# Optimization experiments

Hardware: AMD Instinct MI355X
Metric: run time of the kernel (lower is better)

Reference implementation:

```python
import jax, jax.numpy as jnp
import numpy as np

N_NODES = 100000
N_EDGES = 1600000
IN_CH = 128
OUT_CH = 128

def setup_inputs() -> dict:
    key = jax.random.key(0)
    k1, k2, k3, k4, k5 = jax.random.split(key, 5)
    x = jax.random.normal(k1, (N_NODES, IN_CH), dtype=jnp.float32)
    src = jax.random.randint(k2, (N_EDGES,), 0, N_NODES, dtype=jnp.int64)
    dst = jax.random.randint(k3, (N_EDGES,), 0, N_NODES, dtype=jnp.int64)
    edge_index = jnp.stack([src, dst], axis=0)
    W = jax.random.normal(k4, (OUT_CH, IN_CH), dtype=jnp.float32) * (1.0 / np.sqrt(IN_CH))
    b = jax.random.normal(k5, (OUT_CH,), dtype=jnp.float32) * 0.01
    return {"x": x, "edge_index": edge_index, "W": W, "b": b}

def reference(x, edge_index, W, b):
    n = x.shape[0]
    src, dst = edge_index[0], edge_index[1]
    loop = jnp.arange(n, dtype=edge_index.dtype)
    src_all = jnp.concatenate([src, loop])  # [E+N]
    dst_all = jnp.concatenate([dst, loop])  # [E+N]
    # in-degree (with self loops) per node
    deg = jax.ops.segment_sum(jnp.ones_like(dst_all, dtype=x.dtype), dst_all, num_segments=n)
    norm = (deg[src_all] * deg[dst_all]) ** -0.5
    norm = jnp.where(jnp.isinf(norm), 0.0, norm)
    h = x @ W.T + b  # [N, out_ch]
    msg = h[src_all] * norm[:, None]  # [E+N, out_ch]
    out = jax.ops.segment_sum(msg, dst_all, num_segments=n)  # [N, out_ch]
    return out
```

## Files before the change

### kernel.cpp

```cpp
#include <hip/hip_runtime.h>
#include <hip/hip_bf16.h>


#define N_NODES 100000
#define N_EDGES 1600000
#define CH 128
#define NC 49
#define NBLKA 782
#define CAPC 34816
#define NCHUNK 17
#define NFB 1563
#define FCAP 1280

using bf16x8 = __attribute__((ext_vector_type(8))) short;
using f32x4  = __attribute__((ext_vector_type(4))) float;

__device__ inline unsigned short f2bf(float f) {
    unsigned u = __float_as_uint(f);
    u += 0x7fffu + ((u >> 16) & 1u);
    return (unsigned short)(u >> 16);
}
__device__ inline float bflo(unsigned u) { return __uint_as_float(u << 16); }
__device__ inline float bfhi(unsigned u) { return __uint_as_float(u & 0xffff0000u); }

__global__ __launch_bounds__(256) void k_histA(const int* __restrict__ dst,
                                               int* __restrict__ histG) {
    __shared__ int hist[NC];
    const int t    = threadIdx.x;
    const int base = blockIdx.x * 2048;
    const int n    = min(2048, N_EDGES - base);
    if (t < NC) hist[t] = 0;
    __syncthreads();
#pragma unroll
    for (int h = 0; h < 2; ++h) {
        int idx = h * 1024 + 4 * t;
        if (idx < n) {
            int4 dv = *(const int4*)&dst[base + idx];
            atomicAdd(&hist[dv.x >> 11], 1);
            atomicAdd(&hist[dv.y >> 11], 1);
            atomicAdd(&hist[dv.z >> 11], 1);
            atomicAdd(&hist[dv.w >> 11], 1);
        }
    }
    __syncthreads();
    if (t < NC) histG[(size_t)t * NBLKA + blockIdx.x] = hist[t];
}

__global__ __launch_bounds__(256) void k_scanA(int* __restrict__ histG,
                                               int* __restrict__ ctail) {
    __shared__ int part[256];
    const int k = blockIdx.x;
    int* h = histG + (size_t)k * NBLKA;
    const int t = threadIdx.x;
    const int base = t * 4;
    int a0 = 0, a1 = 0, a2 = 0, a3 = 0;
    if (base + 0 < NBLKA) a0 = h[base + 0];
    if (base + 1 < NBLKA) a1 = h[base + 1];
    if (base + 2 < NBLKA) a2 = h[base + 2];
    if (base + 3 < NBLKA) a3 = h[base + 3];
    const int s = a0 + a1 + a2 + a3;
    part[t] = s;
    __syncthreads();
    for (int off = 1; off < 256; off <<= 1) {
        int x = (t >= off) ? part[t - off] : 0;
        __syncthreads();
        part[t] += x;
        __syncthreads();
    }
    int r = part[t] - s;
    if (t == 255) ctail[k] = part[255];
    if (base + 0 < NBLKA) { h[base + 0] = r; r += a0; }
    if (base + 1 < NBLKA) { h[base + 1] = r; r += a1; }
    if (base + 2 < NBLKA) { h[base + 2] = r; r += a2; }
    if (base + 3 < NBLKA) { h[base + 3] = r; r += a3; }
}

__global__ __launch_bounds__(256) void k_place(const int* __restrict__ src,
                                               const int* __restrict__ dst,
                                               const int* __restrict__ histG,
                                               unsigned* __restrict__ E1) {
    __shared__ int hist[NC];
    __shared__ int boff[NC + 1];
    __shared__ int cur[NC];
    __shared__ int gb[NC];
    __shared__ unsigned stage[2048];
    const int t    = threadIdx.x;
    const int base = blockIdx.x * 2048;
    const int n    = min(2048, N_EDGES - base);

    if (t < NC) {
        hist[t] = 0;
        gb[t] = histG[(size_t)t * NBLKA + blockIdx.x];
    }
    __syncthreads();

    int s[8], d[8];
#pragma unroll
    for (int h = 0; h < 2; ++h) {
        int idx = h * 1024 + 4 * t;
        if (idx < n) {
            int4 sv = *(const int4*)&src[base + idx];
            int4 dv = *(const int4*)&dst[base + idx];
            s[4*h+0] = sv.x; s[4*h+1] = sv.y; s[4*h+2] = sv.z; s[4*h+3] = sv.w;
            d[4*h+0] = dv.x; d[4*h+1] = dv.y; d[4*h+2] = dv.z; d[4*h+3] = dv.w;
        } else {
            d[4*h+0] = d[4*h+1] = d[4*h+2] = d[4*h+3] = -1;
            s[4*h+0] = s[4*h+1] = s[4*h+2] = s[4*h+3] = 0;
        }
    }
#pragma unroll
    for (int j = 0; j < 8; ++j)
        if (d[j] >= 0) atomicAdd(&hist[d[j] >> 11], 1);
    __syncthreads();

    if (t == 0) {
        int run = 0;
        for (int k = 0; k < NC; ++k) { boff[k] = run; run += hist[k]; }
        boff[NC] = run;
    }
    __syncthreads();
    if (t < NC) cur[t] = boff[t];
    __syncthreads();

#pragma unroll
    for (int j = 0; j < 8; ++j)
        if (d[j] >= 0) {
            int k = d[j] >> 11;
            int pos = atomicAdd(&cur[k], 1);
            stage[pos] = ((unsigned)s[j] << 11) | (unsigned)(d[j] & 2047);
        }
    __syncthreads();

    const int tot = boff[NC];
    for (int i = t; i < tot; i += 256) {
        int lo = 0, hi = NC;
#pragma unroll
        for (int it = 0; it < 6; ++it) {
            int mid = (lo + hi) >> 1;
            bool c = (boff[mid] <= i);
            lo = c ? mid : lo;
            hi = c ? hi : mid;
        }
        int p = gb[lo] + (i - boff[lo]);
        if (p < CAPC) E1[(size_t)lo * CAPC + p] = stage[i];
    }
}

__global__ __launch_bounds__(256) void k_sortB(const unsigned* __restrict__ E1,
                                               const int* __restrict__ ctail,
                                               int* __restrict__ ftail,
                                               unsigned* __restrict__ E2) {
    __shared__ int hist[32];
    __shared__ int boff[33];
    __shared__ int cur[32];
    __shared__ int gb[32];
    __shared__ unsigned stage[2048];
    const int cb = blockIdx.x / NCHUNK;
    const int ch = blockIdx.x % NCHUNK;
    const int t  = threadIdx.x;
    int cnt = ctail[cb]; if (cnt > CAPC) cnt = CAPC;
    const int begin = ch * 2048;
    int n = cnt - begin;
    if (n <= 0) return;
    if (n > 2048) n = 2048;
    const unsigned* e1 = E1 + (size_t)cb * CAPC + begin;

    if (t < 32) hist[t] = 0;
    __syncthreads();

    for (int i = t; i < n; i += 256)
        atomicAdd(&hist[(e1[i] >> 6) & 31], 1);
    __syncthreads();

    if (t < 32) gb[t] = atomicAdd(&ftail[cb * 32 + t], hist[t]);
    if (t == 0) {
        int run = 0;
        for (int k = 0; k < 32; ++k) { boff[k] = run; run += hist[k]; }
        boff[32] = run;
    }
    __syncthreads();
    if (t < 32) cur[t] = boff[t];
    __syncthreads();

    for (int i = t; i < n; i += 256) {
        unsigned v = e1[i];
        int k = (v >> 6) & 31;
        int pos = atomicAdd(&cur[k], 1);
        stage[pos] = ((v >> 11) << 6) | (v & 63);
    }
    __syncthreads();

    const int tot = boff[32];
    for (int i = t; i < tot; i += 256) {
        int lo = 0, hi = 32;
#pragma unroll
        for (int it = 0; it < 5; ++it) {
            int mid = (lo + hi) >> 1;
            bool c = (boff[mid] <= i);
            lo = c ? mid : lo;
            hi = c ? hi : mid;
        }
        int p = gb[lo] + (i - boff[lo]);
        int fb = cb * 32 + lo;
        if (p < FCAP) E2[(size_t)fb * FCAP + p] = stage[i];
    }
}

__global__ __launch_bounds__(256) void k_deg(const unsigned* __restrict__ E2,
                                             const int* __restrict__ ftail,
                                             float* __restrict__ rinv) {
    __shared__ int bins[64];
    const int fb = blockIdx.x;
    const int t  = threadIdx.x;
    if (t < 64) bins[t] = 0;
    int n = ftail[fb]; if (n > FCAP) n = FCAP;
    __syncthreads();
    const unsigned* e2 = E2 + (size_t)fb * FCAP;
    for (int i = t; i < n; i += 256) atomicAdd(&bins[e2[i] & 63], 1);
    __syncthreads();
    if (t < 64) {
        int node = fb * 64 + t;
        if (node < N_NODES) rinv[node] = rsqrtf((float)(bins[t] + 1));
    }
}

__device__ inline void cvt8(const float4 a, const float4 b, bf16x8& h, bf16x8& l) {
    bf16x8 H, L;
#define CV(i, f) { unsigned short hb = f2bf(f); H[i] = (short)hb;               \
                   L[i] = (short)f2bf((f) - __uint_as_float((unsigned)hb << 16)); }
    CV(0, a.x) CV(1, a.y) CV(2, a.z) CV(3, a.w)
    CV(4, b.x) CV(5, b.y) CV(6, b.z) CV(7, b.w)
#undef CV
    h = H; l = L;
}

#define MFMA(a, b, c) __builtin_amdgcn_mfma_f32_16x16x32_bf16((a), (b), (c), 0, 0, 0)

__global__ __launch_bounds__(256) void k_gemm(const float* __restrict__ x,
                                              const float* __restrict__ W,
                                              const float* __restrict__ b,
                                              const float* __restrict__ rinv,
                                              unsigned short* __restrict__ hs) {
    __shared__ __align__(16) unsigned short wh[CH * CH];
    __shared__ __align__(16) unsigned short wl[CH * CH];
    const int t = threadIdx.x;

    for (int c = t; c < 2048; c += 256) {
        int o   = c >> 4;
        int kk  = (c & 15) << 3;
        const float* wp = &W[(size_t)o * CH + kk];
        float4 w0 = *(const float4*)wp;
        float4 w1 = *(const float4*)(wp + 4);
        bf16x8 H, L;
        cvt8(w0, w1, H, L);
        unsigned boff = ((unsigned)((o << 8) | (kk << 1))) ^ ((unsigned)(o & 7) << 4);
        *(bf16x8*)((char*)wh + boff) = H;
        *(bf16x8*)((char*)wl + boff) = L;
    }
    __syncthreads();

    const int lane = t & 63;
    const int l15  = lane & 15;
    const int lhi  = lane >> 4;
    const int kc   = lhi << 3;
    const int row_base = blockIdx.x * 128 + (t >> 6) * 32;

    int r0 = row_base + l15;       if (r0 > N_NODES - 1) r0 = N_NODES - 1;
    int r1 = row_base + 16 + l15;  if (r1 > N_NODES - 1) r1 = N_NODES - 1;
    const float* x0 = &x[(size_t)r0 * CH + kc];
    const float* x1 = &x[(size_t)r1 * CH + kc];

    float4 xa[4][2], xb[4][2];
#pragma unroll
    for (int ks = 0; ks < 4; ++ks) {
        xa[ks][0] = *(const float4*)(x0 + ks * 32);
        xa[ks][1] = *(const float4*)(x0 + ks * 32 + 4);
        xb[ks][0] = *(const float4*)(x1 + ks * 32);
        xb[ks][1] = *(const float4*)(x1 + ks * 32 + 4);
    }

    f32x4 acc[2][8];
#pragma unroll
    for (int rf = 0; rf < 2; ++rf)
#pragma unroll
        for (int cf = 0; cf < 8; ++cf)
            acc[rf][cf] = (f32x4){0.f, 0.f, 0.f, 0.f};

#pragma unroll
    for (int ks = 0; ks < 4; ++ks) {
        bf16x8 ah0, al0, ah1, al1;
        cvt8(xa[ks][0], xa[ks][1], ah0, al0);
        cvt8(xb[ks][0], xb[ks][1], ah1, al1);
        const unsigned kb = (unsigned)((ks * 32 + kc) << 1);
#pragma unroll
        for (int cf = 0; cf < 8; ++cf) {
            int o = cf * 16 + l15;
            unsigned boff = (((unsigned)(o << 8)) + kb) ^ ((unsigned)(o & 7) << 4);
            bf16x8 bh = *(const bf16x8*)((const char*)wh + boff);
            bf16x8 bl = *(const bf16x8*)((const char*)wl + boff);
            acc[0][cf] = MFMA(ah0, bh, acc[0][cf]);
            acc[1][cf] = MFMA(ah1, bh, acc[1][cf]);
            acc[0][cf] = MFMA(al0, bh, acc[0][cf]);
            acc[1][cf] = MFMA(al1, bh, acc[1][cf]);
            acc[0][cf] = MFMA(ah0, bl, acc[0][cf]);
            acc[1][cf] = MFMA(ah1, bl, acc[1][cf]);
        }
    }

    float bcol[8];
#pragma unroll
    for (int cf = 0; cf < 8; ++cf) bcol[cf] = b[cf * 16 + l15];

#pragma unroll
    for (int rf = 0; rf < 2; ++rf) {
        int rb = row_base + rf * 16 + lhi * 4;
        if (rb >= N_NODES) continue;
        float4 ri4 = *(const float4*)&rinv[rb];
        float ri[4] = {ri4.x, ri4.y, ri4.z, ri4.w};
#pragma unroll
        for (int j = 0; j < 4; ++j) {
            size_t ro = (size_t)(rb + j) * CH;
#pragma unroll
            for (int cf = 0; cf < 8; ++cf)
                hs[ro + cf * 16 + l15] = f2bf(ri[j] * (acc[rf][cf][j] + bcol[cf]));
        }
    }
}

#define ACC8(u)                                                            \
    do {                                                                   \
        acc[0] += bflo((u).x); acc[1] += bfhi((u).x);                      \
        acc[2] += bflo((u).y); acc[3] += bfhi((u).y);                      \
        acc[4] += bflo((u).z); acc[5] += bfhi((u).z);                      \
        acc[6] += bflo((u).w); acc[7] += bfhi((u).w);                      \
    } while (0)

__global__ __launch_bounds__(256) void k_spmm(const unsigned* __restrict__ E2,
                                              const int* __restrict__ ftail,
                                              const float* __restrict__ rinv,
                                              const unsigned short* __restrict__ hs,
                                              float* __restrict__ out) {
    __shared__ int bins[64];
    __shared__ int boff[65];
    __shared__ int cur[64];
    __shared__ int srt[FCAP];
    const int fb    = blockIdx.x;
    const int node0 = fb * 64;
    const int t     = threadIdx.x;
    const unsigned* e2 = E2 + (size_t)fb * FCAP;
    const uint4* hp = (const uint4*)hs;

    if (t < 64) bins[t] = 0;
    int n = ftail[fb]; if (n > FCAP) n = FCAP;
    __syncthreads();

    for (int i = t; i < n; i += 256) atomicAdd(&bins[e2[i] & 63], 1);
    __syncthreads();

    if (t == 0) {
        int run = 0;
        for (int k = 0; k < 64; ++k) { boff[k] = run; run += bins[k]; }
        boff[64] = run;
    }
    __syncthreads();
    if (t < 64) cur[t] = boff[t];
    __syncthreads();

    for (int i = t; i < n; i += 256) {
        unsigned v = e2[i];
        int pos = atomicAdd(&cur[v & 63], 1);
        srt[pos] = (int)(v >> 6);
    }
    __syncthreads();

    const int grp  = t >> 4;
    const int lane = t & 15;
#pragma unroll
    for (int r = 0; r < 4; ++r) {
        const int nl   = grp * 4 + r;
        const int node = node0 + nl;
        if (node >= N_NODES) continue;
        float acc[8] = {};
        {
            uint4 u = hp[(size_t)node * 16 + lane];
            ACC8(u);
        }
        int e  = boff[nl];
        int e1 = boff[nl + 1];
        for (; e + 8 <= e1; e += 8) {
            int s0 = srt[e + 0], s1 = srt[e + 1], s2 = srt[e + 2], s3 = srt[e + 3];
            int s4 = srt[e + 4], s5 = srt[e + 5], s6 = srt[e + 6], s7 = srt[e + 7];
            uint4 u0 = hp[(size_t)s0 * 16 + lane];
            uint4 u1 = hp[(size_t)s1 * 16 + lane];
            uint4 u2 = hp[(size_t)s2 * 16 + lane];
            uint4 u3 = hp[(size_t)s3 * 16 + lane];
            uint4 u4 = hp[(size_t)s4 * 16 + lane];
            uint4 u5 = hp[(size_t)s5 * 16 + lane];
            uint4 u6 = hp[(size_t)s6 * 16 + lane];
            uint4 u7 = hp[(size_t)s7 * 16 + lane];
            ACC8(u0); ACC8(u1); ACC8(u2); ACC8(u3);
            ACC8(u4); ACC8(u5); ACC8(u6); ACC8(u7);
        }
        for (; e + 4 <= e1; e += 4) {
            int s0 = srt[e + 0];
            int s1 = srt[e + 1];
            int s2 = srt[e + 2];
            int s3 = srt[e + 3];
            uint4 u0 = hp[(size_t)s0 * 16 + lane];
            uint4 u1 = hp[(size_t)s1 * 16 + lane];
            uint4 u2 = hp[(size_t)s2 * 16 + lane];
            uint4 u3 = hp[(size_t)s3 * 16 + lane];
            ACC8(u0); ACC8(u1); ACC8(u2); ACC8(u3);
        }
        for (; e < e1; ++e) {
            uint4 u = hp[(size_t)srt[e] * 16 + lane];
            ACC8(u);
        }
        float ri = rinv[node];
        f32x4 o0, o1;
        o0[0] = ri * acc[0]; o0[1] = ri * acc[1]; o0[2] = ri * acc[2]; o0[3] = ri * acc[3];
        o1[0] = ri * acc[4]; o1[1] = ri * acc[5]; o1[2] = ri * acc[6]; o1[3] = ri * acc[7];
        *(f32x4*)&out[(size_t)node * CH + lane * 8]     = o0;
        *(f32x4*)&out[(size_t)node * CH + lane * 8 + 4] = o1;
    }
}

extern "C" void kernel_launch(void* const* d_in, const int* in_sizes, int n_in,
                              void* d_out, int out_size, void* d_ws, size_t ws_size,
                              hipStream_t stream) {
    const float* x  = (const float*)d_in[0];
    const int*   ei = (const int*)d_in[1];
    const float* W  = (const float*)d_in[2];
    const float* b  = (const float*)d_in[3];
    float* out = (float*)d_out;

    const int* src = ei;
    const int* dst = ei + N_EDGES;

    int*      ctail = (int*)d_ws;
    int*      ftail = ctail + 64;
    int*      histG = ftail + 1600;
    float*    rinv  = (float*)(histG + 38336);
    unsigned* E1    = (unsigned*)(rinv + N_NODES);
    unsigned* E2    = E1 + (size_t)NC * CAPC;
    unsigned short* hs = (unsigned short*)(E2 + (size_t)NFB * FCAP);

    hipMemsetAsync(ftail, 0, 1600 * sizeof(int), stream);

    k_histA<<<NBLKA, 256, 0, stream>>>(dst, histG);
    k_scanA<<<NC, 256, 0, stream>>>(histG, ctail);
    k_place<<<NBLKA, 256, 0, stream>>>(src, dst, histG, E1);
    k_sortB<<<NC * NCHUNK, 256, 0, stream>>>(E1, ctail, ftail, E2);
    k_deg<<<NFB, 256, 0, stream>>>(E2, ftail, rinv);
    k_gemm<<<(N_NODES + 127) / 128, 256, 0, stream>>>(x, W, b, rinv, hs);
    k_spmm<<<NFB, 256, 0, stream>>>(E2, ftail, rinv, hs, out);
}
```

Baseline: 225.1 us.

## Fuse sort pipeline into one cooperative kernel and fold degree computation into consumers

The memset, histogram, scan, place and second-level sort kernels are merged into a single cooperative kernel that uses grid-wide syncs between phases. The separate degree kernel and the rinv buffer are removed: the GEMM recomputes per-node degrees from the bucketed edges, and the SpMM takes them from its existing bins. This saves several launches and the rinv round trip through memory. In exchange it adds grid-sync overhead, requires all 782 blocks to be co-resident, and repeats degree counting in the GEMM.

```diff
diff --git a/kernel.cpp b/kernel.cpp
--- a/kernel.cpp
+++ b/kernel.cpp
@@ -1,5 +1,8 @@
 #include <hip/hip_runtime.h>
 #include <hip/hip_bf16.h>
+#include <hip/hip_cooperative_groups.h>
+
+namespace cg = cooperative_groups;
 
 
 #define N_NODES 100000
@@ -23,12 +26,27 @@
 __device__ inline float bflo(unsigned u) { return __uint_as_float(u << 16); }
 __device__ inline float bfhi(unsigned u) { return __uint_as_float(u & 0xffff0000u); }
 
-__global__ __launch_bounds__(256) void k_histA(const int* __restrict__ dst,
-                                               int* __restrict__ histG) {
+__global__ __launch_bounds__(256) void k_sort(const int* __restrict__ src,
+                                              const int* __restrict__ dst,
+                                              int* __restrict__ ctail,
+                                              int* __restrict__ ftail,
+                                              int* __restrict__ histG,
+                                              unsigned* __restrict__ E1,
+                                              unsigned* __restrict__ E2) {
     __shared__ int hist[NC];
+    __shared__ int boff[NC + 1];
+    __shared__ int cur[NC];
+    __shared__ int gb[NC];
+    __shared__ int part[256];
+    __shared__ unsigned stage[2048];
+    cg::grid_group gg = cg::this_grid();
+
     const int t    = threadIdx.x;
-    const int base = blockIdx.x * 2048;
+    const int bid  = blockIdx.x;
+    const int base = bid * 2048;
     const int n    = min(2048, N_EDGES - base);
+
+    { int i = bid * 256 + t; if (i < 1600) ftail[i] = 0; }
     if (t < NC) hist[t] = 0;
     __syncthreads();
 #pragma unroll
@@ -43,184 +61,153 @@
         }
     }
     __syncthreads();
-    if (t < NC) histG[(size_t)t * NBLKA + blockIdx.x] = hist[t];
-}
-
-__global__ __launch_bounds__(256) void k_scanA(int* __restrict__ histG,
-                                               int* __restrict__ ctail) {
-    __shared__ int part[256];
-    const int k = blockIdx.x;
-    int* h = histG + (size_t)k * NBLKA;
-    const int t = threadIdx.x;
-    const int base = t * 4;
-    int a0 = 0, a1 = 0, a2 = 0, a3 = 0;
-    if (base + 0 < NBLKA) a0 = h[base + 0];
-    if (base + 1 < NBLKA) a1 = h[base + 1];
-    if (base + 2 < NBLKA) a2 = h[base + 2];
-    if (base + 3 < NBLKA) a3 = h[base + 3];
-    const int s = a0 + a1 + a2 + a3;
-    part[t] = s;
-    __syncthreads();
-    for (int off = 1; off < 256; off <<= 1) {
-        int x = (t >= off) ? part[t - off] : 0;
-        __syncthreads();
-        part[t] += x;
-        __syncthreads();
-    }
-    int r = part[t] - s;
-    if (t == 255) ctail[k] = part[255];
-    if (base + 0 < NBLKA) { h[base + 0] = r; r += a0; }
-    if (base + 1 < NBLKA) { h[base + 1] = r; r += a1; }
-    if (base + 2 < NBLKA) { h[base + 2] = r; r += a2; }
-    if (base + 3 < NBLKA) { h[base + 3] = r; r += a3; }
-}
-
-__global__ __launch_bounds__(256) void k_place(const int* __restrict__ src,
-                                               const int* __restrict__ dst,
-                                               const int* __restrict__ histG,
-                                               unsigned* __restrict__ E1) {
-    __shared__ int hist[NC];
-    __shared__ int boff[NC + 1];
-    __shared__ int cur[NC];
-    __shared__ int gb[NC];
-    __shared__ unsigned stage[2048];
-    const int t    = threadIdx.x;
-    const int base = blockIdx.x * 2048;
-    const int n    = min(2048, N_EDGES - base);
-
-    if (t < NC) {
-        hist[t] = 0;
-        gb[t] = histG[(size_t)t * NBLKA + blockIdx.x];
-    }
-    __syncthreads();
-
-    int s[8], d[8];
-#pragma unroll
-    for (int h = 0; h < 2; ++h) {
-        int idx = h * 1024 + 4 * t;
-        if (idx < n) {
-            int4 sv = *(const int4*)&src[base + idx];
-            int4 dv = *(const int4*)&dst[base + idx];
-            s[4*h+0] = sv.x; s[4*h+1] = sv.y; s[4*h+2] = sv.z; s[4*h+3] = sv.w;
-            d[4*h+0] = dv.x; d[4*h+1] = dv.y; d[4*h+2] = dv.z; d[4*h+3] = dv.w;
-        } else {
-            d[4*h+0] = d[4*h+1] = d[4*h+2] = d[4*h+3] = -1;
-            s[4*h+0] = s[4*h+1] = s[4*h+2] = s[4*h+3] = 0;
-        }
-    }
-#pragma unroll
-    for (int j = 0; j < 8; ++j)
-        if (d[j] >= 0) atomicAdd(&hist[d[j] >> 11], 1);
-    __syncthreads();
-
-    if (t == 0) {
-        int run = 0;
-        for (int k = 0; k < NC; ++k) { boff[k] = run; run += hist[k]; }
-        boff[NC] = run;
-    }
-    __syncthreads();
-    if (t < NC) cur[t] = boff[t];
-    __syncthreads();
-
-#pragma unroll
-    for (int j = 0; j < 8; ++j)
-        if (d[j] >= 0) {
-            int k = d[j] >> 11;
+    if (t < NC) histG[(size_t)t * NBLKA + bid] = hist[t];
+
+    __threadfence();
+    gg.sync();
+    __threadfence();
+
+    if (bid < NC) {
+        int* h = histG + (size_t)bid * NBLKA;
+        const int cb4 = t * 4;
+        int a0 = 0, a1 = 0, a2 = 0, a3 = 0;
+        if (cb4 + 0 < NBLKA) a0 = h[cb4 + 0];
+        if (cb4 + 1 < NBLKA) a1 = h[cb4 + 1];
+        if (cb4 + 2 < NBLKA) a2 = h[cb4 + 2];
+        if (cb4 + 3 < NBLKA) a3 = h[cb4 + 3];
+        const int s = a0 + a1 + a2 + a3;
+        part[t] = s;
+        __syncthreads();
+        for (int off = 1; off < 256; off <<= 1) {
+            int x = (t >= off) ? part[t - off] : 0;
+            __syncthreads();
+            part[t] += x;
+            __syncthreads();
+        }
+        int r = part[t] - s;
+        if (t == 255) ctail[bid] = part[255];
+        if (cb4 + 0 < NBLKA) { h[cb4 + 0] = r; r += a0; }
+        if (cb4 + 1 < NBLKA) { h[cb4 + 1] = r; r += a1; }
+        if (cb4 + 2 < NBLKA) { h[cb4 + 2] = r; r += a2; }
+        if (cb4 + 3 < NBLKA) { h[cb4 + 3] = r; r += a3; }
+    }
+
+    __threadfence();
+    gg.sync();
+    __threadfence();
+
+    {
+        if (t < NC) {
+            hist[t] = 0;
+            gb[t] = histG[(size_t)t * NBLKA + bid];
+        }
+        __syncthreads();
+
+        int s[8], d[8];
+#pragma unroll
+        for (int h = 0; h < 2; ++h) {
+            int idx = h * 1024 + 4 * t;
+            if (idx < n) {
+                int4 sv = *(const int4*)&src[base + idx];
+                int4 dv = *(const int4*)&dst[base + idx];
+                s[4*h+0] = sv.x; s[4*h+1] = sv.y; s[4*h+2] = sv.z; s[4*h+3] = sv.w;
+                d[4*h+0] = dv.x; d[4*h+1] = dv.y; d[4*h+2] = dv.z; d[4*h+3] = dv.w;
+            } else {
+                d[4*h+0] = d[4*h+1] = d[4*h+2] = d[4*h+3] = -1;
+                s[4*h+0] = s[4*h+1] = s[4*h+2] = s[4*h+3] = 0;
+            }
+        }
+#pragma unroll
+        for (int j = 0; j < 8; ++j)
+            if (d[j] >= 0) atomicAdd(&hist[d[j] >> 11], 1);
+        __syncthreads();
+
+        if (t == 0) {
+            int run = 0;
+            for (int k = 0; k < NC; ++k) { boff[k] = run; run += hist[k]; }
+            boff[NC] = run;
+        }
+        __syncthreads();
+        if (t < NC) cur[t] = boff[t];
+        __syncthreads();
+
+#pragma unroll
+        for (int j = 0; j < 8; ++j)
+            if (d[j] >= 0) {
+                int k = d[j] >> 11;
+                int pos = atomicAdd(&cur[k], 1);
+                stage[pos] = ((unsigned)s[j] << 11) | (unsigned)(d[j] & 2047);
+            }
+        __syncthreads();
+
+        const int tot = boff[NC];
+        for (int i = t; i < tot; i += 256) {
+            int lo = 0, hi = NC;
+#pragma unroll
+            for (int it = 0; it < 6; ++it) {
+                int mid = (lo + hi) >> 1;
+                bool c = (boff[mid] <= i);
+                lo = c ? mid : lo;
+                hi = c ? hi : mid;
+            }
+            int p = gb[lo] + (i - boff[lo]);
+            if (p < CAPC) E1[(size_t)lo * CAPC + p] = stage[i];
+        }
+    }
+
+    __threadfence();
+    gg.sync();
+    __threadfence();
+
+    for (int u = bid; u < NC * NCHUNK; u += NBLKA) {
+        const int cb = u / NCHUNK;
+        const int ch = u % NCHUNK;
+        int cnt = ctail[cb]; if (cnt > CAPC) cnt = CAPC;
+        const int begin = ch * 2048;
+        int nn = cnt - begin;
+        if (nn <= 0) continue;
+        if (nn > 2048) nn = 2048;
+        const unsigned* e1 = E1 + (size_t)cb * CAPC + begin;
+
+        if (t < 32) hist[t] = 0;
+        __syncthreads();
+        for (int i = t; i < nn; i += 256)
+            atomicAdd(&hist[(e1[i] >> 6) & 31], 1);
+        __syncthreads();
+
+        if (t < 32) gb[t] = atomicAdd(&ftail[cb * 32 + t], hist[t]);
+        if (t == 0) {
+            int run = 0;
+            for (int k = 0; k < 32; ++k) { boff[k] = run; run += hist[k]; }
+            boff[32] = run;
+        }
+        __syncthreads();
+        if (t < 32) cur[t] = boff[t];
+        __syncthreads();
+
+        for (int i = t; i < nn; i += 256) {
+            unsigned v = e1[i];
+            int k = (v >> 6) & 31;
             int pos = atomicAdd(&cur[k], 1);
-            stage[pos] = ((unsigned)s[j] << 11) | (unsigned)(d[j] & 2047);
-        }
-    __syncthreads();
-
-    const int tot = boff[NC];
-    for (int i = t; i < tot; i += 256) {
-        int lo = 0, hi = NC;
-#pragma unroll
-        for (int it = 0; it < 6; ++it) {
-            int mid = (lo + hi) >> 1;
-            bool c = (boff[mid] <= i);
-            lo = c ? mid : lo;
-            hi = c ? hi : mid;
-        }
-        int p = gb[lo] + (i - boff[lo]);
-        if (p < CAPC) E1[(size_t)lo * CAPC + p] = stage[i];
-    }
-}
-
-__global__ __launch_bounds__(256) void k_sortB(const unsigned* __restrict__ E1,
-                                               const int* __restrict__ ctail,
-                                               int* __restrict__ ftail,
-                                               unsigned* __restrict__ E2) {
-    __shared__ int hist[32];
-    __shared__ int boff[33];
-    __shared__ int cur[32];
-    __shared__ int gb[32];
-    __shared__ unsigned stage[2048];
-    const int cb = blockIdx.x / NCHUNK;
-    const int ch = blockIdx.x % NCHUNK;
-    const int t  = threadIdx.x;
-    int cnt = ctail[cb]; if (cnt > CAPC) cnt = CAPC;
-    const int begin = ch * 2048;
-    int n = cnt - begin;
-    if (n <= 0) return;
-    if (n > 2048) n = 2048;
-    const unsigned* e1 = E1 + (size_t)cb * CAPC + begin;
-
-    if (t < 32) hist[t] = 0;
-    __syncthreads();
-
-    for (int i = t; i < n; i += 256)
-        atomicAdd(&hist[(e1[i] >> 6) & 31], 1);
-    __syncthreads();
-
-    if (t < 32) gb[t] = atomicAdd(&ftail[cb * 32 + t], hist[t]);
-    if (t == 0) {
-        int run = 0;
-        for (int k = 0; k < 32; ++k) { boff[k] = run; run += hist[k]; }
-        boff[32] = run;
-    }
-    __syncthreads();
-    if (t < 32) cur[t] = boff[t];
-    __syncthreads();
-
-    for (int i = t; i < n; i += 256) {
-        unsigned v = e1[i];
-        int k = (v >> 6) & 31;
-        int pos = atomicAdd(&cur[k], 1);
-        stage[pos] = ((v >> 11) << 6) | (v & 63);
-    }
-    __syncthreads();
-
-    const int tot = boff[32];
-    for (int i = t; i < tot; i += 256) {
-        int lo = 0, hi = 32;
-#pragma unroll
-        for (int it = 0; it < 5; ++it) {
-            int mid = (lo + hi) >> 1;
-            bool c = (boff[mid] <= i);
-            lo = c ? mid : lo;
-            hi = c ? hi : mid;
-        }
-        int p = gb[lo] + (i - boff[lo]);
-        int fb = cb * 32 + lo;
-        if (p < FCAP) E2[(size_t)fb * FCAP + p] = stage[i];
-    }
-}
-
-__global__ __launch_bounds__(256) void k_deg(const unsigned* __restrict__ E2,
-                                             const int* __restrict__ ftail,
-                                             float* __restrict__ rinv) {
-    __shared__ int bins[64];
-    const int fb = blockIdx.x;
-    const int t  = threadIdx.x;
-    if (t < 64) bins[t] = 0;
-    int n = ftail[fb]; if (n > FCAP) n = FCAP;
-    __syncthreads();
-    const unsigned* e2 = E2 + (size_t)fb * FCAP;
-    for (int i = t; i < n; i += 256) atomicAdd(&bins[e2[i] & 63], 1);
-    __syncthreads();
-    if (t < 64) {
-        int node = fb * 64 + t;
-        if (node < N_NODES) rinv[node] = rsqrtf((float)(bins[t] + 1));
+            stage[pos] = ((v >> 11) << 6) | (v & 63);
+        }
+        __syncthreads();
+
+        const int tot = boff[32];
+        for (int i = t; i < tot; i += 256) {
+            int lo = 0, hi = 32;
+#pragma unroll
+            for (int it = 0; it < 5; ++it) {
+                int mid = (lo + hi) >> 1;
+                bool c = (boff[mid] <= i);
+                lo = c ? mid : lo;
+                hi = c ? hi : mid;
+            }
+            int p = gb[lo] + (i - boff[lo]);
+            int fb = cb * 32 + lo;
+            if (p < FCAP) E2[(size_t)fb * FCAP + p] = stage[i];
+        }
+        __syncthreads();
     }
 }
 
@@ -239,11 +226,41 @@
 __global__ __launch_bounds__(256) void k_gemm(const float* __restrict__ x,
                                               const float* __restrict__ W,
                                               const float* __restrict__ b,
-                                              const float* __restrict__ rinv,
+                                              const unsigned* __restrict__ E2,
+                                              const int* __restrict__ ftail,
                                               unsigned short* __restrict__ hs) {
     __shared__ __align__(16) unsigned short wh[CH * CH];
     __shared__ __align__(16) unsigned short wl[CH * CH];
     const int t = threadIdx.x;
+    const int lane = t & 63;
+    const int l15  = lane & 15;
+    const int lhi  = lane >> 4;
+
+    int* dbin = (int*)wh;
+    if (t < 128) dbin[t] = 0;
+    __syncthreads();
+    {
+        const int fb0 = blockIdx.x * 2;
+        int n0 = ftail[fb0]; if (n0 > FCAP) n0 = FCAP;
+        const unsigned* e0 = E2 + (size_t)fb0 * FCAP;
+        for (int i = t; i < n0; i += 256) atomicAdd(&dbin[e0[i] & 63], 1);
+        const int fb1 = fb0 + 1;
+        if (fb1 < NFB) {
+            int n1 = ftail[fb1]; if (n1 > FCAP) n1 = FCAP;
+            const unsigned* e1p = E2 + (size_t)fb1 * FCAP;
+            for (int i = t; i < n1; i += 256) atomicAdd(&dbin[64 + (e1p[i] & 63)], 1);
+        }
+    }
+    __syncthreads();
+    float rreg[2][4];
+#pragma unroll
+    for (int rf = 0; rf < 2; ++rf) {
+        int lb = (t >> 6) * 32 + rf * 16 + lhi * 4;
+#pragma unroll
+        for (int j = 0; j < 4; ++j)
+            rreg[rf][j] = rsqrtf((float)(dbin[lb + j] + 1));
+    }
+    __syncthreads();
 
     for (int c = t; c < 2048; c += 256) {
         int o   = c >> 4;
@@ -259,10 +276,7 @@
     }
     __syncthreads();
 
-    const int lane = t & 63;
-    const int l15  = lane & 15;
-    const int lhi  = lane >> 4;
-    const int kc   = lhi << 3;
+    const int kc = lhi << 3;
     const int row_base = blockIdx.x * 128 + (t >> 6) * 32;
 
     int r0 = row_base + l15;       if (r0 > N_NODES - 1) r0 = N_NODES - 1;
@@ -315,14 +329,13 @@
     for (int rf = 0; rf < 2; ++rf) {
         int rb = row_base + rf * 16 + lhi * 4;
         if (rb >= N_NODES) continue;
-        float4 ri4 = *(const float4*)&rinv[rb];
-        float ri[4] = {ri4.x, ri4.y, ri4.z, ri4.w};
 #pragma unroll
         for (int j = 0; j < 4; ++j) {
             size_t ro = (size_t)(rb + j) * CH;
+            float ri = rreg[rf][j];
 #pragma unroll
             for (int cf = 0; cf < 8; ++cf)
-                hs[ro + cf * 16 + l15] = f2bf(ri[j] * (acc[rf][cf][j] + bcol[cf]));
+                hs[ro + cf * 16 + l15] = f2bf(ri * (acc[rf][cf][j] + bcol[cf]));
         }
     }
 }
@@ -337,7 +350,6 @@
 
 __global__ __launch_bounds__(256) void k_spmm(const unsigned* __restrict__ E2,
                                               const int* __restrict__ ftail,
-                                              const float* __restrict__ rinv,
                                               const unsigned short* __restrict__ hs,
                                               float* __restrict__ out) {
     __shared__ int bins[64];
@@ -416,7 +428,7 @@
             uint4 u = hp[(size_t)srt[e] * 16 + lane];
             ACC8(u);
         }
-        float ri = rinv[node];
+        float ri = rsqrtf((float)(bins[nl] + 1));
         f32x4 o0, o1;
         o0[0] = ri * acc[0]; o0[1] = ri * acc[1]; o0[2] = ri * acc[2]; o0[3] = ri * acc[3];
         o1[0] = ri * acc[4]; o1[1] = ri * acc[5]; o1[2] = ri * acc[6]; o1[3] = ri * acc[7];
@@ -434,24 +446,20 @@
     const float* b  = (const float*)d_in[3];
     float* out = (float*)d_out;
 
-    const int* src = ei;
-    const int* dst = ei + N_EDGES;
+    const int* src = (const int*)ei;
+    const int* dst = (const int*)ei + N_EDGES;
 
     int*      ctail = (int*)d_ws;
     int*      ftail = ctail + 64;
     int*      histG = ftail + 1600;
-    float*    rinv  = (float*)(histG + 38336);
-    unsigned* E1    = (unsigned*)(rinv + N_NODES);
+    unsigned* E1    = (unsigned*)(histG + 38336);
     unsigned* E2    = E1 + (size_t)NC * CAPC;
     unsigned short* hs = (unsigned short*)(E2 + (size_t)NFB * FCAP);
 
-    hipMemsetAsync(ftail, 0, 1600 * sizeof(int), stream);
-
-    k_histA<<<NBLKA, 256, 0, stream>>>(dst, histG);
-    k_scanA<<<NC, 256, 0, stream>>>(histG, ctail);
-    k_place<<<NBLKA, 256, 0, stream>>>(src, dst, histG, E1);
-    k_sortB<<<NC * NCHUNK, 256, 0, stream>>>(E1, ctail, ftail, E2);
-    k_deg<<<NFB, 256, 0, stream>>>(E2, ftail, rinv);
-    k_gemm<<<(N_NODES + 127) / 128, 256, 0, stream>>>(x, W, b, rinv, hs);
-    k_spmm<<<NFB, 256, 0, stream>>>(E2, ftail, rinv, hs, out);
-}
+    void* args[] = {(void*)&src, (void*)&dst, (void*)&ctail, (void*)&ftail,
+                    (void*)&histG, (void*)&E1, (void*)&E2};
+    (void)hipLaunchCooperativeKernel((void*)k_sort, dim3(NBLKA), dim3(256),
+                                     args, 0, stream);
+    k_gemm<<<NBLKA, 256, 0, stream>>>(x, W, b, E2, ftail, hs);
+    k_spmm<<<NFB, 256, 0, stream>>>(E2, ftail, hs, out);
+}
```

Result: slower. 762.9 us (+238.9%).

## Fuse degree computation into gemm and spmm, fold memset into histogram kernel

Applied to the files above, without the earlier changes.

Removes the separate k_deg kernel and the rinv buffer. Each gemm block now histograms the two 64-node E2 buckets that cover its 128 rows, using the W staging shared memory, and spmm recomputes rsqrt from its own bins. The ftail zeroing moves from a memset into k_histA. This cuts two launches and a global round trip, at the cost of extra edge reads and shared atomics in front of the gemm.

```diff
diff --git a/kernel.cpp b/kernel.cpp
--- a/kernel.cpp
+++ b/kernel.cpp
@@ -24,11 +24,13 @@
 __device__ inline float bfhi(unsigned u) { return __uint_as_float(u & 0xffff0000u); }
 
 __global__ __launch_bounds__(256) void k_histA(const int* __restrict__ dst,
-                                               int* __restrict__ histG) {
+                                               int* __restrict__ histG,
+                                               int* __restrict__ ftail) {
     __shared__ int hist[NC];
     const int t    = threadIdx.x;
     const int base = blockIdx.x * 2048;
     const int n    = min(2048, N_EDGES - base);
+    { int i = blockIdx.x * 256 + t; if (i < 1600) ftail[i] = 0; }
     if (t < NC) hist[t] = 0;
     __syncthreads();
 #pragma unroll
@@ -206,24 +208,6 @@
     }
 }
 
-__global__ __launch_bounds__(256) void k_deg(const unsigned* __restrict__ E2,
-                                             const int* __restrict__ ftail,
-                                             float* __restrict__ rinv) {
-    __shared__ int bins[64];
-    const int fb = blockIdx.x;
-    const int t  = threadIdx.x;
-    if (t < 64) bins[t] = 0;
-    int n = ftail[fb]; if (n > FCAP) n = FCAP;
-    __syncthreads();
-    const unsigned* e2 = E2 + (size_t)fb * FCAP;
-    for (int i = t; i < n; i += 256) atomicAdd(&bins[e2[i] & 63], 1);
-    __syncthreads();
-    if (t < 64) {
-        int node = fb * 64 + t;
-        if (node < N_NODES) rinv[node] = rsqrtf((float)(bins[t] + 1));
-    }
-}
-
 __device__ inline void cvt8(const float4 a, const float4 b, bf16x8& h, bf16x8& l) {
     bf16x8 H, L;
 #define CV(i, f) { unsigned short hb = f2bf(f); H[i] = (short)hb;               \
@@ -239,11 +223,41 @@
 __global__ __launch_bounds__(256) void k_gemm(const float* __restrict__ x,
                                               const float* __restrict__ W,
                                               const float* __restrict__ b,
-                                              const float* __restrict__ rinv,
+                                              const unsigned* __restrict__ E2,
+                                              const int* __restrict__ ftail,
                                               unsigned short* __restrict__ hs) {
     __shared__ __align__(16) unsigned short wh[CH * CH];
     __shared__ __align__(16) unsigned short wl[CH * CH];
     const int t = threadIdx.x;
+    const int lane = t & 63;
+    const int l15  = lane & 15;
+    const int lhi  = lane >> 4;
+
+    int* dbin = (int*)wh;
+    if (t < 128) dbin[t] = 0;
+    __syncthreads();
+    {
+        const int fb0 = blockIdx.x * 2;
+        int n0 = ftail[fb0]; if (n0 > FCAP) n0 = FCAP;
+        const unsigned* e0 = E2 + (size_t)fb0 * FCAP;
+        for (int i = t; i < n0; i += 256) atomicAdd(&dbin[e0[i] & 63], 1);
+        const int fb1 = fb0 + 1;
+        if (fb1 < NFB) {
+            int n1 = ftail[fb1]; if (n1 > FCAP) n1 = FCAP;
+            const unsigned* e1p = E2 + (size_t)fb1 * FCAP;
+            for (int i = t; i < n1; i += 256) atomicAdd(&dbin[64 + (e1p[i] & 63)], 1);
+        }
+    }
+    __syncthreads();
+    float rreg[2][4];
+#pragma unroll
+    for (int rf = 0; rf < 2; ++rf) {
+        int lb = (t >> 6) * 32 + rf * 16 + lhi * 4;
+#pragma unroll
+        for (int j = 0; j < 4; ++j)
+            rreg[rf][j] = rsqrtf((float)(dbin[lb + j] + 1));
+    }
+    __syncthreads();
 
     for (int c = t; c < 2048; c += 256) {
         int o   = c >> 4;
@@ -259,10 +273,7 @@
     }
     __syncthreads();
 
-    const int lane = t & 63;
-    const int l15  = lane & 15;
-    const int lhi  = lane >> 4;
-    const int kc   = lhi << 3;
+    const int kc = lhi << 3;
     const int row_base = blockIdx.x * 128 + (t >> 6) * 32;
 
     int r0 = row_base + l15;       if (r0 > N_NODES - 1) r0 = N_NODES - 1;
@@ -315,14 +326,13 @@
     for (int rf = 0; rf < 2; ++rf) {
         int rb = row_base + rf * 16 + lhi * 4;
         if (rb >= N_NODES) continue;
-        float4 ri4 = *(const float4*)&rinv[rb];
-        float ri[4] = {ri4.x, ri4.y, ri4.z, ri4.w};
 #pragma unroll
         for (int j = 0; j < 4; ++j) {
             size_t ro = (size_t)(rb + j) * CH;
+            float ri = rreg[rf][j];
 #pragma unroll
             for (int cf = 0; cf < 8; ++cf)
-                hs[ro + cf * 16 + l15] = f2bf(ri[j] * (acc[rf][cf][j] + bcol[cf]));
+                hs[ro + cf * 16 + l15] = f2bf(ri * (acc[rf][cf][j] + bcol[cf]));
         }
     }
 }
@@ -337,7 +347,6 @@
 
 __global__ __launch_bounds__(256) void k_spmm(const unsigned* __restrict__ E2,
                                               const int* __restrict__ ftail,
-                                              const float* __restrict__ rinv,
                                               const unsigned short* __restrict__ hs,
                                               float* __restrict__ out) {
     __shared__ int bins[64];
@@ -416,7 +425,7 @@
             uint4 u = hp[(size_t)srt[e] * 16 + lane];
             ACC8(u);
         }
-        float ri = rinv[node];
+        float ri = rsqrtf((float)(bins[nl] + 1));
         f32x4 o0, o1;
         o0[0] = ri * acc[0]; o0[1] = ri * acc[1]; o0[2] = ri * acc[2]; o0[3] = ri * acc[3];
         o1[0] = ri * acc[4]; o1[1] = ri * acc[5]; o1[2] = ri * acc[6]; o1[3] = ri * acc[7];
@@ -434,24 +443,20 @@
     const float* b  = (const float*)d_in[3];
     float* out = (float*)d_out;
 
-    const int* src = ei;
-    const int* dst = ei + N_EDGES;
+    const int* src = (const int*)ei;
+    const int* dst = (const int*)ei + N_EDGES;
 
     int*      ctail = (int*)d_ws;
     int*      ftail = ctail + 64;
     int*      histG = ftail + 1600;
-    float*    rinv  = (float*)(histG + 38336);
-    unsigned* E1    = (unsigned*)(rinv + N_NODES);
+    unsigned* E1    = (unsigned*)(histG + 38336);
     unsigned* E2    = E1 + (size_t)NC * CAPC;
     unsigned short* hs = (unsigned short*)(E2 + (size_t)NFB * FCAP);
 
-    hipMemsetAsync(ftail, 0, 1600 * sizeof(int), stream);
-
-    k_histA<<<NBLKA, 256, 0, stream>>>(dst, histG);
+    k_histA<<<NBLKA, 256, 0, stream>>>(dst, histG, ftail);
     k_scanA<<<NC, 256, 0, stream>>>(histG, ctail);
     k_place<<<NBLKA, 256, 0, stream>>>(src, dst, histG, E1);
     k_sortB<<<NC * NCHUNK, 256, 0, stream>>>(E1, ctail, ftail, E2);
-    k_deg<<<NFB, 256, 0, stream>>>(E2, ftail, rinv);
-    k_gemm<<<(N_NODES + 127) / 128, 256, 0, stream>>>(x, W, b, rinv, hs);
-    k_spmm<<<NFB, 256, 0, stream>>>(E2, ftail, rinv, hs, out);
-}
+    k_gemm<<<NBLKA, 256, 0, stream>>>(x, W, b, E2, ftail, hs);
+    k_spmm<<<NFB, 256, 0, stream>>>(E2, ftail, hs, out);
+}
```

Result: no change. 221.9 us (-1.4%).
